# Performance work log

Measured on AMD Instinct MI355X. Metric: run time of the kernel, lower is better.

## Reference

```python
import jax, jax.numpy as jnp
import numpy as np

B, C, T = 8, 1024, 2048
CI = C // 2
BN_EPS = 1e-5


def setup_inputs() -> dict:
    key = jax.random.key(0)
    ks = jax.random.split(key, 12)
    sc_in = 1.0 / np.sqrt(C)
    sc_ci = 1.0 / np.sqrt(CI)
    return {
        "x": jax.random.normal(ks[0], (B, C, T), dtype=jnp.float32),
        "Wq_w": jax.random.normal(ks[1], (CI, C), dtype=jnp.float32) * sc_in,
        "Wq_b": jax.random.normal(ks[2], (CI,), dtype=jnp.float32) * 0.02,
        "Wk_w": jax.random.normal(ks[3], (CI, C), dtype=jnp.float32) * sc_in,
        "Wk_b": jax.random.normal(ks[4], (CI,), dtype=jnp.float32) * 0.02,
        "Wv_w": jax.random.normal(ks[5], (CI, C), dtype=jnp.float32) * sc_in,
        "Wv_b": jax.random.normal(ks[6], (CI,), dtype=jnp.float32) * 0.02,
        "Wo_w": jax.random.normal(ks[7], (C, CI), dtype=jnp.float32) * sc_ci,
        "Wo_b": jax.random.normal(ks[8], (C,), dtype=jnp.float32) * 0.02,
        "gamma": jax.random.normal(ks[9], (C,), dtype=jnp.float32) * 0.1 + 1.0,
        "beta": jax.random.normal(ks[10], (C,), dtype=jnp.float32) * 0.02,
    }


def reference(x, Wq_w, Wq_b, Wk_w, Wk_b, Wv_w, Wv_b, Wo_w, Wo_b, gamma, beta):
    # 1x1 Conv1d projections == channel-wise linear maps
    q = jnp.einsum('oc,bct->bto', Wq_w, x) + Wq_b          # [B, T, Ci]
    k = jnp.einsum('oc,bct->bot', Wk_w, x) + Wk_b[:, None]  # [B, Ci, T]
    v = jnp.einsum('oc,bct->bto', Wv_w, x) + Wv_b          # [B, T, Ci]

    s = jnp.einsum('bqc,bck->bqk', q, k)                   # [B, Tq, Tk], unscaled
    sim = jax.nn.softmax(s, axis=-2)                        # softmax over QUERY axis
    y = jnp.einsum('bqk,bkc->bcq', sim, v)                  # [B, Ci, T]

    wy = jnp.einsum('oc,bct->bot', Wo_w, y) + Wo_b[:, None]  # [B, C, T]

    # BatchNorm1d in training mode: stats over (batch, time) per channel
    mean = jnp.mean(wy, axis=(0, 2), keepdims=True)
    var = jnp.var(wy, axis=(0, 2), keepdims=True)
    wy_bn = (wy - mean) * jax.lax.rsqrt(var + BN_EPS)
    wy_bn = wy_bn * gamma[None, :, None] + beta[None, :, None]

    return wy_bn + x
```

## Files before the change

kernel.cpp:

```cpp
#include <hip/hip_runtime.h>
#include <hip/hip_fp16.h>

typedef _Float16 f16;
typedef f16 f16x8 __attribute__((ext_vector_type(8)));
typedef f16 f16x4 __attribute__((ext_vector_type(4)));
typedef float f32x4 __attribute__((ext_vector_type(4)));

constexpr int Bb = 8, Cc = 1024, Tt = 2048, Ci = 512;
constexpr float BN_EPS = 1e-5f;

__device__ __forceinline__ void gload16(const f16* g, f16* l) {
  __builtin_amdgcn_global_load_lds(
      (const __attribute__((address_space(1))) void*)g,
      (__attribute__((address_space(3))) void*)l, 16, 0, 0);
}

__global__ __launch_bounds__(256)
void cvt_kernel(const float* __restrict__ src, f16* __restrict__ dst, int n4) {
  int i = blockIdx.x * blockDim.x + threadIdx.x;
  if (i < n4) {
    float4 v = *((const float4*)src + i);
    f16x4 h;
    h[0] = (f16)v.x; h[1] = (f16)v.y; h[2] = (f16)v.z; h[3] = (f16)v.w;
    *((f16x4*)dst + i) = h;
  }
}

__global__ __launch_bounds__(256)
void cvtT_kernel(const float* __restrict__ x, f16* __restrict__ xT) {
  __shared__ float tile[64][68];
  const int b = blockIdx.z, c0 = blockIdx.y * 64, t0 = blockIdx.x * 64;
  const int tid = threadIdx.x;
  const float* xp = x + ((long)b * Cc + c0) * Tt + t0;
  {
    int r = tid >> 4, c4 = (tid & 15) * 4;
    #pragma unroll
    for (int it = 0; it < 4; it++) {
      float4 v = *(const float4*)(xp + (long)(r + it * 16) * Tt + c4);
      *(float4*)&tile[r + it * 16][c4] = v;
    }
  }
  __syncthreads();
  f16* op = xT + ((long)b * Tt + t0) * Cc + c0;
  {
    int c8 = (tid & 7) * 8;
    #pragma unroll
    for (int it = 0; it < 2; it++) {
      int t = (tid >> 3) + it * 32;
      f16x8 o;
      #pragma unroll
      for (int jj = 0; jj < 8; jj++) o[jj] = (f16)tile[c8 + jj][t];
      *(f16x8*)(op + (long)t * Cc + c8) = o;
    }
  }
}

template<int BIAS_MODE>
__global__ __launch_bounds__(512, 2)
void gemm8p(const f16* __restrict__ A, const f16* __restrict__ B,
            f16* __restrict__ C, const float* __restrict__ bias,
            int K, int lda, int ldb, int ldc, long sA, long sB, long sC)
{
  extern __shared__ f16 lds[];
  constexpr int TILE_A = 256 * 64;
  constexpr int TILE_B = 128 * 64;
  constexpr int TILE   = TILE_A + TILE_B;

  const int tid = threadIdx.x, lane = tid & 63, wv = tid >> 6;
  const int bm0 = blockIdx.y * 256, bn0 = blockIdx.x * 128;
  const int wm = (wv >> 1) * 64, wn = (wv & 1) * 64;
  const f16* Ab = A + (long)blockIdx.z * sA + (long)bm0 * lda;
  const f16* Bt = B + (long)blockIdx.z * sB + (long)bn0 * ldb;
  C += (long)blockIdx.z * sC;

  const int r16 = lane & 15, khi = lane >> 4;
  const int sw = (r16 & 7) << 4;

  auto stA = [&](int slot, int k0, int r) {
    int L = (r * 512 + tid) * 16;
    int G = L ^ (((L >> 7) & 7) << 4);
    gload16(Ab + (long)(G >> 7) * lda + k0 + ((G & 127) >> 1),
            lds + (long)slot * TILE + (r * 512 + wv * 64) * 8);
  };
  auto stB = [&](int slot, int k0, int r) {
    int L = (r * 512 + tid) * 16;
    int G = L ^ (((L >> 7) & 7) << 4);
    gload16(Bt + (long)(G >> 7) * ldb + k0 + ((G & 127) >> 1),
            lds + (long)slot * TILE + TILE_A + (r * 512 + wv * 64) * 8);
  };

  f32x4 acc[4][4] = {};
  const int nt = K >> 6;

  #pragma unroll
  for (int r = 0; r < 4; r++) stA(0, 0, r);
  #pragma unroll
  for (int r = 0; r < 2; r++) stB(0, 0, r);
  #pragma unroll
  for (int r = 0; r < 4; r++) stA(1, 64, r);
  #pragma unroll
  for (int r = 0; r < 2; r++) stB(1, 64, r);
  asm volatile("s_waitcnt vmcnt(6)" ::: "memory");
  __builtin_amdgcn_s_barrier();

  for (int t = 0; t < nt; t++) {
    const int slot = t % 3;
    const int nslot = (t + 2) % 3;
    const int k2 = (t + 2) << 6;
    const bool st = (t + 2) < nt;
    const char* baseA = (const char*)(lds + (long)slot * TILE);
    const char* baseB = (const char*)(lds + (long)slot * TILE + TILE_A);

    if (st) {
      stA(nslot, k2, 0); stA(nslot, k2, 1); stA(nslot, k2, 2); stA(nslot, k2, 3);
      stB(nslot, k2, 0); stB(nslot, k2, 1);
    }

    f16x8 af0[4], bf0[4], af1[4], bf1[4];
    #pragma unroll
    for (int mi = 0; mi < 4; mi++)
      af0[mi] = *(const f16x8*)(baseA + (((wm + mi * 16 + r16) * 128 + khi * 16) ^ sw));
    #pragma unroll
    for (int nj = 0; nj < 4; nj++)
      bf0[nj] = *(const f16x8*)(baseB + (((wn + nj * 16 + r16) * 128 + khi * 16) ^ sw));
    #pragma unroll
    for (int mi = 0; mi < 4; mi++)
      af1[mi] = *(const f16x8*)(baseA + (((wm + mi * 16 + r16) * 128 + 64 + khi * 16) ^ sw));
    #pragma unroll
    for (int nj = 0; nj < 4; nj++)
      bf1[nj] = *(const f16x8*)(baseB + (((wn + nj * 16 + r16) * 128 + 64 + khi * 16) ^ sw));

    __builtin_amdgcn_s_setprio(1);
    #pragma unroll
    for (int mi = 0; mi < 4; mi++)
      #pragma unroll
      for (int nj = 0; nj < 4; nj++)
        acc[mi][nj] = __builtin_amdgcn_mfma_f32_16x16x32_f16(af0[mi], bf0[nj], acc[mi][nj], 0, 0, 0);
    #pragma unroll
    for (int mi = 0; mi < 4; mi++)
      #pragma unroll
      for (int nj = 0; nj < 4; nj++)
        acc[mi][nj] = __builtin_amdgcn_mfma_f32_16x16x32_f16(af1[mi], bf1[nj], acc[mi][nj], 0, 0, 0);
    __builtin_amdgcn_s_setprio(0);

    __builtin_amdgcn_sched_barrier(0);
    if (st) asm volatile("s_waitcnt vmcnt(6)" ::: "memory");
    else    asm volatile("s_waitcnt vmcnt(0)" ::: "memory");
    __builtin_amdgcn_s_barrier();
  }

  const int rg = khi * 4;
  #pragma unroll
  for (int mi = 0; mi < 4; mi++) {
    const int row = bm0 + wm + mi * 16 + rg;
    #pragma unroll
    for (int nj = 0; nj < 4; nj++) {
      const int col = bn0 + wn + nj * 16 + r16;
      const float bn_ = (BIAS_MODE == 2) ? bias[col] : 0.0f;
      #pragma unroll
      for (int r = 0; r < 4; r++) {
        float v = acc[mi][nj][r] + ((BIAS_MODE == 1) ? bias[row + r] : bn_);
        C[(long)(row + r) * ldc + col] = (f16)v;
      }
    }
  }
}

__global__ __launch_bounds__(256)
void rowstat_kernel(const f16* __restrict__ S, float* __restrict__ maxs,
                    float* __restrict__ sums) {
  __shared__ float red[8];
  const int tid = threadIdx.x;
  const f16* p = S + (long)blockIdx.x * Tt;
  f16x8 v = *((const f16x8*)p + tid);
  float f[8];
  float mx = -3e38f;
  #pragma unroll
  for (int j = 0; j < 8; j++) { f[j] = (float)v[j]; mx = fmaxf(mx, f[j]); }
  #pragma unroll
  for (int off = 1; off < 64; off <<= 1) mx = fmaxf(mx, __shfl_xor(mx, off));
  const int w = tid >> 6;
  if ((tid & 63) == 0) red[w] = mx;
  __syncthreads();
  mx = fmaxf(fmaxf(red[0], red[1]), fmaxf(red[2], red[3]));
  float sum = 0.f;
  #pragma unroll
  for (int j = 0; j < 8; j++) sum += __expf(f[j] - mx);
  #pragma unroll
  for (int off = 1; off < 64; off <<= 1) sum += __shfl_xor(sum, off);
  __syncthreads();
  if ((tid & 63) == 0) red[4 + w] = sum;
  __syncthreads();
  if (tid == 0) {
    maxs[blockIdx.x] = mx;
    sums[blockIdx.x] = (red[4] + red[5]) + (red[6] + red[7]);
  }
}

__global__ __launch_bounds__(256)
void transnorm_kernel(const f16* __restrict__ St, const float* __restrict__ maxs,
                      const float* __restrict__ sums, f16* __restrict__ P) {
  __shared__ f16 tile[64][72];
  __shared__ float rm[64], ri[64];
  const int b = blockIdx.z, kt0 = blockIdx.y * 64, q0 = blockIdx.x * 64;
  const int tid = threadIdx.x;
  if (tid < 64) {
    rm[tid] = maxs[(long)b * Tt + kt0 + tid];
    ri[tid] = 1.0f / sums[(long)b * Tt + kt0 + tid];
  }
  const f16* Sp = St + ((long)b * Tt + kt0) * Tt + q0;
  {
    int r = tid >> 3, c8 = (tid & 7) * 8;
    #pragma unroll
    for (int it = 0; it < 2; it++) {
      f16x8 v = *(const f16x8*)(Sp + (long)(r + it * 32) * Tt + c8);
      *(f16x8*)&tile[r + it * 32][c8] = v;
    }
  }
  __syncthreads();
  f16* Pp = P + ((long)b * Tt + q0) * Tt + kt0;
  {
    int kt8 = (tid & 7) * 8;
    #pragma unroll
    for (int it = 0; it < 2; it++) {
      int q = (tid >> 3) + it * 32;
      f16x8 o;
      #pragma unroll
      for (int jj = 0; jj < 8; jj++) {
        int kt = kt8 + jj;
        o[jj] = (f16)(__expf((float)tile[kt][q] - rm[kt]) * ri[kt]);
      }
      *(f16x8*)(Pp + (long)q * Tt + kt8) = o;
    }
  }
}

__global__ __launch_bounds__(256)
void bnstat_kernel(const f16* __restrict__ wy, float* __restrict__ bsum,
                   float* __restrict__ bsq) {
  const int c = blockIdx.x, tid = threadIdx.x;
  float s1 = 0.f, s2 = 0.f;
  for (int b = 0; b < Bb; b++) {
    f16x8 v = *((const f16x8*)(wy + ((long)b * Cc + c) * Tt) + tid);
    #pragma unroll
    for (int jj = 0; jj < 8; jj++) { float f = (float)v[jj]; s1 += f; s2 += f * f; }
  }
  #pragma unroll
  for (int off = 1; off < 64; off <<= 1) {
    s1 += __shfl_xor(s1, off);
    s2 += __shfl_xor(s2, off);
  }
  __shared__ float l1[4], l2[4];
  const int w = tid >> 6;
  if ((tid & 63) == 0) { l1[w] = s1; l2[w] = s2; }
  __syncthreads();
  if (tid == 0) {
    bsum[c] = (l1[0] + l1[1]) + (l1[2] + l1[3]);
    bsq[c]  = (l2[0] + l2[1]) + (l2[2] + l2[3]);
  }
}

__global__ __launch_bounds__(256)
void final_kernel(const f16* __restrict__ wy, const float* __restrict__ x,
                  const float* __restrict__ gamma, const float* __restrict__ beta,
                  const float* __restrict__ bsum, const float* __restrict__ bsq,
                  float* __restrict__ out)
{
  long i = ((long)blockIdx.x * blockDim.x + threadIdx.x) * 4;
  int c = (int)((i >> 11) & (Cc - 1));
  const float cnt = (float)Bb * (float)Tt;
  float mean = bsum[c] / cnt;
  float var  = bsq[c] / cnt - mean * mean;
  float sc = rsqrtf(var + BN_EPS) * gamma[c];
  float sh = beta[c] - mean * sc;
  f16x4 w = *(const f16x4*)(wy + i);
  float4 xv = *(const float4*)(x + i);
  float4 o;
  o.x = (float)w[0] * sc + sh + xv.x;
  o.y = (float)w[1] * sc + sh + xv.y;
  o.z = (float)w[2] * sc + sh + xv.z;
  o.w = (float)w[3] * sc + sh + xv.w;
  *(float4*)(out + i) = o;
}

extern "C" void kernel_launch(void* const* d_in, const int* in_sizes, int n_in,
                              void* d_out, int out_size, void* d_ws, size_t ws_size,
                              hipStream_t stream) {
  const float* x    = (const float*)d_in[0];
  const float* Wq_w = (const float*)d_in[1];
  const float* Wq_b = (const float*)d_in[2];
  const float* Wk_w = (const float*)d_in[3];
  const float* Wk_b = (const float*)d_in[4];
  const float* Wv_w = (const float*)d_in[5];
  const float* Wv_b = (const float*)d_in[6];
  const float* Wo_w = (const float*)d_in[7];
  const float* Wo_b = (const float*)d_in[8];
  const float* gamma = (const float*)d_in[9];
  const float* beta  = (const float*)d_in[10];
  float* out = (float*)d_out;

  constexpr long SZ_XT = (long)Bb * Tt * Cc;
  constexpr long SZ_Q  = (long)Bb * Tt * Ci;
  constexpr long SZ_S  = (long)Bb * Tt * Tt;
  constexpr long SZ_W  = (long)Ci * Cc;

  f16* ws = (f16*)d_ws;
  f16* xT = ws;
  f16* P  = ws;
  f16* Qm = ws + SZ_XT;
  f16* Km = Qm + SZ_Q;
  f16* Vt = Km + SZ_Q;
  f16* St = Vt + SZ_Q;
  f16* wq = St + SZ_S;
  f16* wk = wq + SZ_W;
  f16* wv = wk + SZ_W;
  f16* wo = wv + SZ_W;
  f16* Y  = wo + SZ_W;
  f16* wy = Y + SZ_Q;
  float* maxs = (float*)(wy + SZ_XT);
  float* sums = maxs + (long)Bb * Tt;
  float* bsum = sums + (long)Bb * Tt;
  float* bsq  = bsum + Cc;

  constexpr int LDSB = (256 * 64 + 128 * 64) * 3 * 2;
  hipFuncSetAttribute(reinterpret_cast<const void*>(gemm8p<0>),
                      hipFuncAttributeMaxDynamicSharedMemorySize, LDSB);
  hipFuncSetAttribute(reinterpret_cast<const void*>(gemm8p<1>),
                      hipFuncAttributeMaxDynamicSharedMemorySize, LDSB);
  hipFuncSetAttribute(reinterpret_cast<const void*>(gemm8p<2>),
                      hipFuncAttributeMaxDynamicSharedMemorySize, LDSB);

  cvt_kernel<<<(int)(SZ_W / 4 / 256), 256, 0, stream>>>(Wq_w, wq, (int)(SZ_W / 4));
  cvt_kernel<<<(int)(SZ_W / 4 / 256), 256, 0, stream>>>(Wk_w, wk, (int)(SZ_W / 4));
  cvt_kernel<<<(int)(SZ_W / 4 / 256), 256, 0, stream>>>(Wv_w, wv, (int)(SZ_W / 4));
  cvt_kernel<<<(int)(SZ_W / 4 / 256), 256, 0, stream>>>(Wo_w, wo, (int)(SZ_W / 4));
  cvtT_kernel<<<dim3(Tt / 64, Cc / 64, Bb), 256, 0, stream>>>(x, xT);

  gemm8p<2><<<dim3(Ci / 128, Tt / 256, Bb), 512, LDSB, stream>>>(
      xT, wq, Qm, Wq_b, Cc, Cc, Cc, Ci, (long)Tt * Cc, 0, (long)Tt * Ci);
  gemm8p<2><<<dim3(Ci / 128, Tt / 256, Bb), 512, LDSB, stream>>>(
      xT, wk, Km, Wk_b, Cc, Cc, Cc, Ci, (long)Tt * Cc, 0, (long)Tt * Ci);
  gemm8p<1><<<dim3(Tt / 128, Ci / 256, Bb), 512, LDSB, stream>>>(
      wv, xT, Vt, Wv_b, Cc, Cc, Cc, Tt, 0, (long)Tt * Cc, (long)Ci * Tt);

  gemm8p<0><<<dim3(Tt / 128, Tt / 256, Bb), 512, LDSB, stream>>>(
      Km, Qm, St, nullptr, Ci, Ci, Ci, Tt, (long)Tt * Ci, (long)Tt * Ci, (long)Tt * Tt);

  rowstat_kernel<<<Bb * Tt, 256, 0, stream>>>(St, maxs, sums);
  transnorm_kernel<<<dim3(Tt / 64, Tt / 64, Bb), 256, 0, stream>>>(St, maxs, sums, P);

  gemm8p<0><<<dim3(Ci / 128, Tt / 256, Bb), 512, LDSB, stream>>>(
      P, Vt, Y, nullptr, Tt, Tt, Tt, Ci, (long)Tt * Tt, (long)Ci * Tt, (long)Tt * Ci);

  gemm8p<1><<<dim3(Tt / 128, Cc / 256, Bb), 512, LDSB, stream>>>(
      wo, Y, wy, Wo_b, Ci, Ci, Ci, Tt, 0, (long)Tt * Ci, (long)Cc * Tt);

  bnstat_kernel<<<Cc, 256, 0, stream>>>(wy, bsum, bsq);
  final_kernel<<<(int)(SZ_XT / 4 / 256), 256, 0, stream>>>(
      wy, x, gamma, beta, bsum, bsq, out);
}
```

Baseline: 300.6 us.

## Add 256x256 GEMM kernel, fuse Q/K projections, reorder gemm8p MFMA fragments

Adds a new 256x256-tile double-buffered GEMM kernel that interleaves its global-to-LDS loads with MFMA clusters in four phases. It is used for a fused Q+K projection (one GEMM over concatenated weights), the QK^T score GEMM and the output projection. The gemm8p kernel also regroups its accumulators into 32x32 quadrants to change fragment load order and register use. The aim is higher operand reuse per tile and fewer launches, at the cost of more registers and LDS per block. The new kernel has no LDS swizzle, so it risks bank conflicts.

```diff
diff --git a/kernel.cpp b/kernel.cpp
--- a/kernel.cpp
+++ b/kernel.cpp
@@ -51,6 +51,124 @@
       #pragma unroll
       for (int jj = 0; jj < 8; jj++) o[jj] = (f16)tile[c8 + jj][t];
       *(f16x8*)(op + (long)t * Cc + c8) = o;
+    }
+  }
+}
+
+#define SYNC_LDS() \
+  __builtin_amdgcn_s_barrier(); \
+  asm volatile("s_waitcnt lgkmcnt(0)" ::: "memory"); \
+  __builtin_amdgcn_sched_barrier(0);
+
+#define MFMA_CLUSTER(AH) \
+  __builtin_amdgcn_s_setprio(1); \
+  _Pragma("unroll") \
+  for (int mi = 0; mi < 4; mi++) { \
+    _Pragma("unroll") \
+    for (int nj = 0; nj < 4; nj++) \
+      acc[(AH)*4 + mi][nj] = __builtin_amdgcn_mfma_f32_16x16x32_f16( \
+          af[mi], bf[nj], acc[(AH)*4 + mi][nj], 0, 0, 0); \
+  } \
+  __builtin_amdgcn_s_setprio(0);
+
+template<int BIAS_MODE>
+__global__ __launch_bounds__(512, 2)
+void gemm256(const f16* __restrict__ A, const f16* __restrict__ B,
+             f16* __restrict__ C, const float* __restrict__ bias,
+             const float* __restrict__ bias2,
+             int K, int lda, int ldb, int ldc, long sA, long sB, long sC)
+{
+  extern __shared__ f16 lds[];
+  const int tid = threadIdx.x, lane = tid & 63, wv = tid >> 6;
+  const int bm0 = blockIdx.y * 256, bn0 = blockIdx.x * 256;
+  const int wm = wv >> 2, wn = wv & 3;
+  const f16* Ab = A + blockIdx.z * sA + (long)bm0 * lda;
+  const f16* Bt = B + blockIdx.z * sB + (long)bn0 * ldb;
+  C += blockIdx.z * sC;
+  const int r16 = lane & 15, khi4 = lane >> 4;
+  const int trow = tid & 255, tkq = tid >> 8;
+
+  auto stA = [&](int nsel, int q, int k0) {
+    gload16(Ab + (long)trow * lda + k0 + (2 * q + tkq) * 8,
+            lds + nsel * 32768 + (q * 512 + wv * 64) * 8);
+  };
+  auto stB = [&](int nsel, int q, int k0) {
+    gload16(Bt + (long)trow * ldb + k0 + (2 * q + tkq) * 8,
+            lds + nsel * 32768 + 16384 + (q * 512 + wv * 64) * 8);
+  };
+
+  f32x4 acc[8][4] = {};
+  const int nt = K >> 6;
+  const int aoff = (khi4 * 256 + wm * 128 + r16) * 8;
+  const int boff = (khi4 * 256 + wn * 64 + r16) * 8;
+
+  stA(0, 0, 0); stA(0, 1, 0);
+  stB(0, 0, 0); stB(0, 1, 0);
+  stA(0, 2, 0); stA(0, 3, 0);
+  stB(0, 2, 0); stB(0, 3, 0);
+  asm volatile("s_waitcnt vmcnt(4)" ::: "memory");
+  __builtin_amdgcn_s_barrier();
+  __builtin_amdgcn_sched_barrier(0);
+
+  for (int t = 0; t < nt; t++) {
+    const int bsel = t & 1, nsel = bsel ^ 1, kn = (t + 1) << 6;
+    const bool st = (t + 1) < nt;
+    const f16* lA = lds + bsel * 32768;
+    const f16* lB = lA + 16384;
+    f16x8 af[4], bf[4];
+
+    if (st) { stA(nsel, 0, kn); stA(nsel, 1, kn); }
+    #pragma unroll
+    for (int mi = 0; mi < 4; mi++) af[mi] = *(const f16x8*)(lA + aoff + mi * 128);
+    #pragma unroll
+    for (int nj = 0; nj < 4; nj++) bf[nj] = *(const f16x8*)(lB + boff + nj * 128);
+    SYNC_LDS();
+    MFMA_CLUSTER(0);
+    __builtin_amdgcn_s_barrier();
+
+    if (st) { stB(nsel, 0, kn); stB(nsel, 1, kn); }
+    #pragma unroll
+    for (int mi = 0; mi < 4; mi++) af[mi] = *(const f16x8*)(lA + aoff + 512 + mi * 128);
+    SYNC_LDS();
+    MFMA_CLUSTER(1);
+    if (st) asm volatile("s_waitcnt vmcnt(4)" ::: "memory");
+    else    asm volatile("s_waitcnt vmcnt(0)" ::: "memory");
+    __builtin_amdgcn_s_barrier();
+    __builtin_amdgcn_sched_barrier(0);
+
+    if (st) { stA(nsel, 2, kn); stA(nsel, 3, kn); }
+    #pragma unroll
+    for (int mi = 0; mi < 4; mi++) af[mi] = *(const f16x8*)(lA + aoff + 8192 + mi * 128);
+    #pragma unroll
+    for (int nj = 0; nj < 4; nj++) bf[nj] = *(const f16x8*)(lB + boff + 8192 + nj * 128);
+    SYNC_LDS();
+    MFMA_CLUSTER(0);
+    __builtin_amdgcn_s_barrier();
+
+    if (st) { stB(nsel, 2, kn); stB(nsel, 3, kn); }
+    #pragma unroll
+    for (int mi = 0; mi < 4; mi++) af[mi] = *(const f16x8*)(lA + aoff + 8704 + mi * 128);
+    SYNC_LDS();
+    MFMA_CLUSTER(1);
+    if (st) asm volatile("s_waitcnt vmcnt(4)" ::: "memory");
+    __builtin_amdgcn_s_barrier();
+    __builtin_amdgcn_sched_barrier(0);
+  }
+
+  const int rg = khi4 * 4;
+  #pragma unroll
+  for (int i = 0; i < 8; i++) {
+    const int row = bm0 + wm * 128 + (i >> 2) * 64 + (i & 3) * 16 + rg;
+    #pragma unroll
+    for (int nj = 0; nj < 4; nj++) {
+      const int col = bn0 + wn * 64 + nj * 16 + r16;
+      float bn_ = 0.0f;
+      if (BIAS_MODE == 2) bn_ = (col < 512) ? bias[col] : bias2[col - 512];
+      #pragma unroll
+      for (int r = 0; r < 4; r++) {
+        float v = acc[i][nj][r] + ((BIAS_MODE == 1) ? bias[row + r] : bn_);
+        C[(long)(row + r) * ldc + col] = (f16)v;
+      }
     }
   }
 }
@@ -89,7 +207,7 @@
             lds + (long)slot * TILE + TILE_A + (r * 512 + wv * 64) * 8);
   };
 
-  f32x4 acc[4][4] = {};
+  f32x4 acc[2][2][4] = {};
   const int nt = K >> 6;
 
   #pragma unroll
@@ -116,31 +234,37 @@
       stB(nslot, k2, 0); stB(nslot, k2, 1);
     }
 
-    f16x8 af0[4], bf0[4], af1[4], bf1[4];
-    #pragma unroll
-    for (int mi = 0; mi < 4; mi++)
-      af0[mi] = *(const f16x8*)(baseA + (((wm + mi * 16 + r16) * 128 + khi * 16) ^ sw));
-    #pragma unroll
-    for (int nj = 0; nj < 4; nj++)
-      bf0[nj] = *(const f16x8*)(baseB + (((wn + nj * 16 + r16) * 128 + khi * 16) ^ sw));
-    #pragma unroll
-    for (int mi = 0; mi < 4; mi++)
-      af1[mi] = *(const f16x8*)(baseA + (((wm + mi * 16 + r16) * 128 + 64 + khi * 16) ^ sw));
-    #pragma unroll
-    for (int nj = 0; nj < 4; nj++)
-      bf1[nj] = *(const f16x8*)(baseB + (((wn + nj * 16 + r16) * 128 + 64 + khi * 16) ^ sw));
+    f16x8 af0[2], bf0[2], af1[2], bf1[2];
+    #pragma unroll
+    for (int i = 0; i < 2; i++) {
+      af0[i] = *(const f16x8*)(baseA + (((wm + i * 16 + 32 * 0 + r16) * 128 + khi * 16) ^ sw));
+      af1[i] = *(const f16x8*)(baseA + (((wm + i * 16 + r16) * 128 + 64 + khi * 16) ^ sw));
+      bf0[i] = *(const f16x8*)(baseB + (((wn + i * 16 + r16) * 128 + khi * 16) ^ sw));
+      bf1[i] = *(const f16x8*)(baseB + (((wn + i * 16 + r16) * 128 + 64 + khi * 16) ^ sw));
+    }
+    f16x8 af0b[2], bf0b[2], af1b[2], bf1b[2];
+    #pragma unroll
+    for (int i = 0; i < 2; i++) {
+      af0b[i] = *(const f16x8*)(baseA + (((wm + 32 + i * 16 + r16) * 128 + khi * 16) ^ sw));
+      af1b[i] = *(const f16x8*)(baseA + (((wm + 32 + i * 16 + r16) * 128 + 64 + khi * 16) ^ sw));
+      bf0b[i] = *(const f16x8*)(baseB + (((wn + 32 + i * 16 + r16) * 128 + khi * 16) ^ sw));
+      bf1b[i] = *(const f16x8*)(baseB + (((wn + 32 + i * 16 + r16) * 128 + 64 + khi * 16) ^ sw));
+    }
 
     __builtin_amdgcn_s_setprio(1);
     #pragma unroll
-    for (int mi = 0; mi < 4; mi++)
+    for (int i = 0; i < 2; i++)
       #pragma unroll
-      for (int nj = 0; nj < 4; nj++)
-        acc[mi][nj] = __builtin_amdgcn_mfma_f32_16x16x32_f16(af0[mi], bf0[nj], acc[mi][nj], 0, 0, 0);
-    #pragma unroll
-    for (int mi = 0; mi < 4; mi++)
-      #pragma unroll
-      for (int nj = 0; nj < 4; nj++)
-        acc[mi][nj] = __builtin_amdgcn_mfma_f32_16x16x32_f16(af1[mi], bf1[nj], acc[mi][nj], 0, 0, 0);
+      for (int j = 0; j < 2; j++) {
+        acc[i][j][0] = __builtin_amdgcn_mfma_f32_16x16x32_f16(af0[i], bf0[j], acc[i][j][0], 0, 0, 0);
+        acc[i][j][0] = __builtin_amdgcn_mfma_f32_16x16x32_f16(af1[i], bf1[j], acc[i][j][0], 0, 0, 0);
+        acc[i][j][1] = __builtin_amdgcn_mfma_f32_16x16x32_f16(af0[i], bf0b[j], acc[i][j][1], 0, 0, 0);
+        acc[i][j][1] = __builtin_amdgcn_mfma_f32_16x16x32_f16(af1[i], bf1b[j], acc[i][j][1], 0, 0, 0);
+        acc[i][j][2] = __builtin_amdgcn_mfma_f32_16x16x32_f16(af0b[i], bf0[j], acc[i][j][2], 0, 0, 0);
+        acc[i][j][2] = __builtin_amdgcn_mfma_f32_16x16x32_f16(af1b[i], bf1[j], acc[i][j][2], 0, 0, 0);
+        acc[i][j][3] = __builtin_amdgcn_mfma_f32_16x16x32_f16(af0b[i], bf0b[j], acc[i][j][3], 0, 0, 0);
+        acc[i][j][3] = __builtin_amdgcn_mfma_f32_16x16x32_f16(af1b[i], bf1b[j], acc[i][j][3], 0, 0, 0);
+      }
     __builtin_amdgcn_s_setprio(0);
 
     __builtin_amdgcn_sched_barrier(0);
@@ -151,19 +275,20 @@
 
   const int rg = khi * 4;
   #pragma unroll
-  for (int mi = 0; mi < 4; mi++) {
-    const int row = bm0 + wm + mi * 16 + rg;
-    #pragma unroll
-    for (int nj = 0; nj < 4; nj++) {
-      const int col = bn0 + wn + nj * 16 + r16;
-      const float bn_ = (BIAS_MODE == 2) ? bias[col] : 0.0f;
+  for (int i = 0; i < 2; i++)
+    #pragma unroll
+    for (int j = 0; j < 2; j++)
       #pragma unroll
-      for (int r = 0; r < 4; r++) {
-        float v = acc[mi][nj][r] + ((BIAS_MODE == 1) ? bias[row + r] : bn_);
-        C[(long)(row + r) * ldc + col] = (f16)v;
+      for (int q = 0; q < 4; q++) {
+        const int row = bm0 + wm + (q >> 1) * 32 + i * 16 + rg;
+        const int col = bn0 + wn + (q & 1) * 32 + j * 16 + r16;
+        const float bn_ = (BIAS_MODE == 2) ? bias[col] : 0.0f;
+        #pragma unroll
+        for (int r = 0; r < 4; r++) {
+          float v = acc[i][j][q][r] + ((BIAS_MODE == 1) ? bias[row + r] : bn_);
+          C[(long)(row + r) * ldc + col] = (f16)v;
+        }
       }
-    }
-  }
 }
 
 __global__ __launch_bounds__(256)
@@ -307,13 +432,11 @@
   f16* ws = (f16*)d_ws;
   f16* xT = ws;
   f16* P  = ws;
-  f16* Qm = ws + SZ_XT;
-  f16* Km = Qm + SZ_Q;
-  f16* Vt = Km + SZ_Q;
+  f16* QK = ws + SZ_XT;
+  f16* Vt = QK + 2 * SZ_Q;
   f16* St = Vt + SZ_Q;
-  f16* wq = St + SZ_S;
-  f16* wk = wq + SZ_W;
-  f16* wv = wk + SZ_W;
+  f16* wqk = St + SZ_S;
+  f16* wv = wqk + 2 * SZ_W;
   f16* wo = wv + SZ_W;
   f16* Y  = wo + SZ_W;
   f16* wy = Y + SZ_Q;
@@ -322,38 +445,45 @@
   float* bsum = sums + (long)Bb * Tt;
   float* bsq  = bsum + Cc;
 
-  constexpr int LDSB = (256 * 64 + 128 * 64) * 3 * 2;
+  constexpr int LDSB256 = 2 * 32768 * 2;
+  constexpr int LDSB8P  = (256 * 64 + 128 * 64) * 3 * 2;
+  hipFuncSetAttribute(reinterpret_cast<const void*>(gemm256<0>),
+                      hipFuncAttributeMaxDynamicSharedMemorySize, LDSB256);
+  hipFuncSetAttribute(reinterpret_cast<const void*>(gemm256<1>),
+                      hipFuncAttributeMaxDynamicSharedMemorySize, LDSB256);
+  hipFuncSetAttribute(reinterpret_cast<const void*>(gemm256<2>),
+                      hipFuncAttributeMaxDynamicSharedMemorySize, LDSB256);
   hipFuncSetAttribute(reinterpret_cast<const void*>(gemm8p<0>),
-                      hipFuncAttributeMaxDynamicSharedMemorySize, LDSB);
+                      hipFuncAttributeMaxDynamicSharedMemorySize, LDSB8P);
   hipFuncSetAttribute(reinterpret_cast<const void*>(gemm8p<1>),
-                      hipFuncAttributeMaxDynamicSharedMemorySize, LDSB);
-  hipFuncSetAttribute(reinterpret_cast<const void*>(gemm8p<2>),
-                      hipFuncAttributeMaxDynamicSharedMemorySize, LDSB);
-
-  cvt_kernel<<<(int)(SZ_W / 4 / 256), 256, 0, stream>>>(Wq_w, wq, (int)(SZ_W / 4));
-  cvt_kernel<<<(int)(SZ_W / 4 / 256), 256, 0, stream>>>(Wk_w, wk, (int)(SZ_W / 4));
+                      hipFuncAttributeMaxDynamicSharedMemorySize, LDSB8P);
+
+  cvt_kernel<<<(int)(SZ_W / 4 / 256), 256, 0, stream>>>(Wq_w, wqk, (int)(SZ_W / 4));
+  cvt_kernel<<<(int)(SZ_W / 4 / 256), 256, 0, stream>>>(Wk_w, wqk + SZ_W, (int)(SZ_W / 4));
   cvt_kernel<<<(int)(SZ_W / 4 / 256), 256, 0, stream>>>(Wv_w, wv, (int)(SZ_W / 4));
   cvt_kernel<<<(int)(SZ_W / 4 / 256), 256, 0, stream>>>(Wo_w, wo, (int)(SZ_W / 4));
   cvtT_kernel<<<dim3(Tt / 64, Cc / 64, Bb), 256, 0, stream>>>(x, xT);
 
-  gemm8p<2><<<dim3(Ci / 128, Tt / 256, Bb), 512, LDSB, stream>>>(
-      xT, wq, Qm, Wq_b, Cc, Cc, Cc, Ci, (long)Tt * Cc, 0, (long)Tt * Ci);
-  gemm8p<2><<<dim3(Ci / 128, Tt / 256, Bb), 512, LDSB, stream>>>(
-      xT, wk, Km, Wk_b, Cc, Cc, Cc, Ci, (long)Tt * Cc, 0, (long)Tt * Ci);
-  gemm8p<1><<<dim3(Tt / 128, Ci / 256, Bb), 512, LDSB, stream>>>(
+  gemm256<2><<<dim3(1024 / 256, Tt / 256, Bb), 512, LDSB256, stream>>>(
+      xT, wqk, QK, Wq_b, Wk_b,
+      Cc, Cc, Cc, 1024, (long)Tt * Cc, 0, (long)Tt * 1024);
+
+  gemm8p<1><<<dim3(Tt / 128, Ci / 256, Bb), 512, LDSB8P, stream>>>(
       wv, xT, Vt, Wv_b, Cc, Cc, Cc, Tt, 0, (long)Tt * Cc, (long)Ci * Tt);
 
-  gemm8p<0><<<dim3(Tt / 128, Tt / 256, Bb), 512, LDSB, stream>>>(
-      Km, Qm, St, nullptr, Ci, Ci, Ci, Tt, (long)Tt * Ci, (long)Tt * Ci, (long)Tt * Tt);
+  gemm256<0><<<dim3(Tt / 256, Tt / 256, Bb), 512, LDSB256, stream>>>(
+      QK + 512, QK, St, nullptr, nullptr,
+      Ci, 1024, 1024, Tt, (long)Tt * 1024, (long)Tt * 1024, (long)Tt * Tt);
 
   rowstat_kernel<<<Bb * Tt, 256, 0, stream>>>(St, maxs, sums);
   transnorm_kernel<<<dim3(Tt / 64, Tt / 64, Bb), 256, 0, stream>>>(St, maxs, sums, P);
 
-  gemm8p<0><<<dim3(Ci / 128, Tt / 256, Bb), 512, LDSB, stream>>>(
+  gemm8p<0><<<dim3(Ci / 128, Tt / 256, Bb), 512, LDSB8P, stream>>>(
       P, Vt, Y, nullptr, Tt, Tt, Tt, Ci, (long)Tt * Tt, (long)Ci * Tt, (long)Tt * Ci);
 
-  gemm8p<1><<<dim3(Tt / 128, Cc / 256, Bb), 512, LDSB, stream>>>(
-      wo, Y, wy, Wo_b, Ci, Ci, Ci, Tt, 0, (long)Tt * Ci, (long)Cc * Tt);
+  gemm256<1><<<dim3(Tt / 256, Cc / 256, Bb), 512, LDSB256, stream>>>(
+      wo, Y, wy, Wo_b, nullptr,
+      Ci, Ci, Ci, Tt, 0, (long)Tt * Ci, (long)Cc * Tt);
 
   bnstat_kernel<<<Cc, 256, 0, stream>>>(wy, bsum, bsq);
   final_kernel<<<(int)(SZ_XT / 4 / 256), 256, 0, stream>>>(
```

After: 314.5 us. 1.05x slower.
